# Performance work log

Measured on AMD Instinct MI355X. Metric: run time of the kernel, lower is better.

## Reference

```python
import jax, jax.numpy as jnp
import numpy as np

N, E, G = 50000, 400000, 2000
H, HEADS, HD = 128, 4, 32


def setup_inputs() -> dict:
    key = jax.random.key(0)
    ks = jax.random.split(key, 16)
    nrm = lambda k, shape, s=0.05: jax.random.normal(k, shape, dtype=jnp.float32) * s
    inp = {}
    inp["x"] = jax.random.normal(ks[0], (N, 39), dtype=jnp.float32)
    inp["edge_index"] = jax.random.randint(ks[1], (2, E), 0, N, dtype=jnp.int32)
    inp["edge_attr"] = jax.random.normal(ks[2], (E, 8), dtype=jnp.float32)
    inp["batch"] = jnp.sort(jax.random.randint(ks[3], (N,), 0, G, dtype=jnp.int32))
    inp["in_W"] = nrm(ks[4], (39, H)); inp["in_b"] = jnp.zeros((H,), jnp.float32)
    inp["in_g"] = jnp.ones((H,), jnp.float32); inp["in_beta"] = jnp.zeros((H,), jnp.float32)
    inp["Wl"] = nrm(ks[5], (3, H, H)); inp["Wr"] = nrm(ks[6], (3, H, H))
    inp["We"] = nrm(ks[7], (3, 8, H)); inp["att"] = nrm(ks[8], (3, HEADS, HD))
    inp["conv_b"] = jnp.zeros((3, H), jnp.float32)
    inp["bn_g"] = jnp.ones((3, H), jnp.float32); inp["bn_b"] = jnp.zeros((3, H), jnp.float32)
    inp["t1_W"] = nrm(ks[9], (3 * H, 256)); inp["t1_b"] = jnp.zeros((256,), jnp.float32)
    inp["t1_g"] = jnp.ones((256,), jnp.float32); inp["t1_beta"] = jnp.zeros((256,), jnp.float32)
    inp["t2_W"] = nrm(ks[10], (256, 128)); inp["t2_b"] = jnp.zeros((128,), jnp.float32)
    inp["t2_g"] = jnp.ones((128,), jnp.float32); inp["t2_beta"] = jnp.zeros((128,), jnp.float32)
    inp["head_W"] = nrm(ks[11], (128, 12)); inp["head_b"] = jnp.zeros((12,), jnp.float32)
    return inp


def _bn(h, g, b):
    # BatchNorm1d in training mode: normalize with batch statistics.
    m = h.mean(0)
    v = ((h - m) ** 2).mean(0)
    return g * (h - m) * jax.lax.rsqrt(v + 1e-5) + b


def reference(x, edge_index, edge_attr, batch, in_W, in_b, in_g, in_beta,
              Wl, Wr, We, att, conv_b, bn_g, bn_b,
              t1_W, t1_b, t1_g, t1_beta, t2_W, t2_b, t2_g, t2_beta,
              head_W, head_b):
    src, dst = edge_index[0], edge_index[1]  # messages flow src -> dst (PyG convention)
    xn = jax.nn.relu(_bn(x @ in_W + in_b, in_g, in_beta))  # [N, H]
    for l in range(3):  # three residual GATv2 layers
        xl = (xn @ Wl[l]).reshape(N, HEADS, HD)  # lin_l (source transform)
        xr = (xn @ Wr[l]).reshape(N, HEADS, HD)  # lin_r (target transform)
        ep = (edge_attr @ We[l]).reshape(E, HEADS, HD)
        m = jax.nn.leaky_relu(xl[src] + xr[dst] + ep, 0.2)  # [E, HEADS, HD]
        alpha = jnp.einsum('ehd,hd->eh', m, att[l])  # [E, HEADS]
        amax = jax.ops.segment_max(alpha, dst, num_segments=N)
        amax = jnp.where(jnp.isfinite(amax), amax, 0.0)  # nodes with no in-edges
        ae = jnp.exp(alpha - amax[dst])
        denom = jax.ops.segment_sum(ae, dst, num_segments=N)
        a = ae / (denom[dst] + 1e-16)  # scatter-softmax over neighborhoods
        agg = jax.ops.segment_sum(xl[src] * a[:, :, None], dst, num_segments=N)
        h = agg.reshape(N, H) + conv_b[l]
        h = jax.nn.elu(_bn(h, bn_g[l], bn_b[l]))
        xn = xn + h
    # 3-way global pooling per graph
    cnt = jax.ops.segment_sum(jnp.ones((N,), jnp.float32), batch, num_segments=G)
    sadd = jax.ops.segment_sum(xn, batch, num_segments=G)
    smean = sadd / jnp.maximum(cnt, 1.0)[:, None]
    smax = jax.ops.segment_max(xn, batch, num_segments=G)
    smax = jnp.where(cnt[:, None] > 0, smax, 0.0)
    xg = jnp.concatenate([smean, smax, sadd], axis=1)  # [G, 3H]
    t = jax.nn.relu(_bn(xg @ t1_W + t1_b, t1_g, t1_beta))
    t = jax.nn.relu(_bn(t @ t2_W + t2_b, t2_g, t2_beta))
    return jax.nn.sigmoid(t @ head_W + head_b)  # [G, 12]
```

## Files before the change

### kernel.cpp

```cpp
#include <hip/hip_runtime.h>
#include <math.h>


constexpr int N_ = 50000;
constexpr int E_ = 400000;
constexpr int G_ = 2000;
constexpr int H_ = 128;
constexpr int IN_ = 39;

typedef __attribute__((ext_vector_type(8))) short bf16x8;
typedef __attribute__((ext_vector_type(4))) float f32x4;

__device__ __forceinline__ unsigned pk_bf16(float a, float b) {
  unsigned ua = __float_as_uint(a);
  unsigned ub = __float_as_uint(b);
  ua = (ua + 0x7fffu + ((ua >> 16) & 1u)) >> 16;
  ub = (ub + 0x7fffu + ((ub >> 16) & 1u)) & 0xffff0000u;
  return ua | ub;
}
__device__ __forceinline__ unsigned short bf16_1(float x) {
  unsigned u = __float_as_uint(x);
  u = (u + 0x7fffu + ((u >> 16) & 1u)) >> 16;
  return (unsigned short)u;
}
__device__ __forceinline__ float up_lo(unsigned u) { return __uint_as_float(u << 16); }
__device__ __forceinline__ float up_hi(unsigned u) { return __uint_as_float(u & 0xffff0000u); }

__global__ __launch_bounds__(256) void hist_kernel(const int* __restrict__ keys, int n,
                                                   int* __restrict__ cnt) {
  for (int i = blockIdx.x * 256 + threadIdx.x; i < n; i += gridDim.x * 256)
    atomicAdd(&cnt[keys[i]], 1);
}

__global__ __launch_bounds__(1024) void scan_local(const int* __restrict__ in,
                                                   int* __restrict__ outx,
                                                   int* __restrict__ bsum, int n) {
  __shared__ int wsum[16];
  int t = threadIdx.x, lane = t & 63, wid = t >> 6;
  int idx = blockIdx.x * 1024 + t;
  int v = (idx < n) ? in[idx] : 0;
  int x = v;
#pragma unroll
  for (int off = 1; off < 64; off <<= 1) {
    int y = __shfl_up(x, off, 64);
    if (lane >= off) x += y;
  }
  if (lane == 63) wsum[wid] = x;
  __syncthreads();
  if (t == 0) {
    int acc = 0;
#pragma unroll
    for (int w = 0; w < 16; w++) { int tmp = wsum[w]; wsum[w] = acc; acc += tmp; }
    bsum[blockIdx.x] = acc;
  }
  __syncthreads();
  if (idx < n) outx[idx] = wsum[wid] + x - v;
}

__global__ __launch_bounds__(64) void scan_bsum(const int* __restrict__ bsum,
                                                int* __restrict__ boff, int nb) {
  int t = threadIdx.x;
  int v = (t < nb) ? bsum[t] : 0;
  int x = v;
#pragma unroll
  for (int off = 1; off < 64; off <<= 1) {
    int y = __shfl_up(x, off, 64);
    if (t >= off) x += y;
  }
  boff[t] = x - v;
}

__global__ __launch_bounds__(1024) void scan_add(int* __restrict__ eoff,
                                                 const int* __restrict__ boff,
                                                 int* __restrict__ cursor, int n) {
  int idx = blockIdx.x * 1024 + threadIdx.x;
  if (idx < n) {
    int e = eoff[idx] + boff[idx >> 10];
    eoff[idx] = e;
    cursor[idx] = e;
  }
  if (idx == 0) eoff[n] = E_;
}

__global__ __launch_bounds__(256) void goff_from_sorted(const int* __restrict__ batch,
                                                        int* __restrict__ goff) {
  int i = blockIdx.x * 256 + threadIdx.x;
  if (i >= N_) return;
  int bi = batch[i];
  int bp = (i == 0) ? -1 : batch[i - 1];
  for (int g = bp + 1; g <= bi; g++) goff[g] = i;
  if (i == N_ - 1) {
    for (int g = bi + 1; g <= G_; g++) goff[g] = N_;
  }
}

__global__ __launch_bounds__(256) void edge_scatter(const int* __restrict__ ei,
                                                    const float* __restrict__ ea,
                                                    int* __restrict__ cursor,
                                                    int* __restrict__ esrc,
                                                    unsigned* __restrict__ easb) {
  int e = blockIdx.x * 256 + threadIdx.x;
  if (e >= E_) return;
  int src = ei[e];
  int dst = ei[E_ + e];
  int j = atomicAdd(&cursor[dst], 1);
  esrc[j] = src;
  const float4* eav = (const float4*)(ea + (size_t)e * 8);
  float4 a0 = eav[0], a1 = eav[1];
  uint4 o;
  o.x = pk_bf16(a0.x, a0.y);
  o.y = pk_bf16(a0.z, a0.w);
  o.z = pk_bf16(a1.x, a1.y);
  o.w = pk_bf16(a1.z, a1.w);
  ((uint4*)easb)[j] = o;
}

__global__ __launch_bounds__(256) void pack_weights(const float* __restrict__ Wl,
                                                    const float* __restrict__ Wr,
                                                    unsigned short* __restrict__ wpack) {
  int i = blockIdx.x * 256 + threadIdx.x;
  if (i >= 3 * 128 * 256) return;
  int l = i >> 15;
  int rem = i & 32767;
  int k = rem >> 8;
  int n = rem & 255;
  const float* Wsrc = (n < 128) ? (Wl + l * H_ * H_) : (Wr + l * H_ * H_);
  int nn = n & 127;
  wpack[(size_t)l * 32768 + n * 128 + k] = bf16_1(Wsrc[k * H_ + nn]);
}

__global__ __launch_bounds__(256) void in_gemm(const float* __restrict__ x,
                                               const float* __restrict__ W,
                                               const float* __restrict__ b,
                                               float* __restrict__ y,
                                               float* __restrict__ ssum,
                                               float* __restrict__ ssq) {
  __shared__ float xs[32][40];
  __shared__ float s1[256], s2[256];
  int t = threadIdx.x;
  int row0 = blockIdx.x * 32;
  for (int i = t; i < 32 * IN_; i += 256) {
    int r = i / IN_, k = i % IN_;
    int row = row0 + r;
    xs[r][k] = (row < N_) ? x[row * IN_ + k] : 0.f;
  }
  __syncthreads();
  int col = t & 127;
  int half = t >> 7;
  float acc[16];
#pragma unroll
  for (int r = 0; r < 16; r++) acc[r] = 0.f;
  for (int k = 0; k < IN_; k++) {
    float w = W[k * H_ + col];
#pragma unroll
    for (int r = 0; r < 16; r++) acc[r] = fmaf(xs[half * 16 + r][k], w, acc[r]);
  }
  float bb = b[col];
  float a1 = 0.f, a2 = 0.f;
#pragma unroll
  for (int r = 0; r < 16; r++) {
    int row = row0 + half * 16 + r;
    float v = acc[r] + bb;
    if (row < N_) {
      y[row * H_ + col] = v;
      a1 += v;
      a2 = fmaf(v, v, a2);
    }
  }
  s1[t] = a1; s2[t] = a2;
  __syncthreads();
  if (t < 128) {
    atomicAdd(&ssum[t], s1[t] + s1[t + 128]);
    atomicAdd(&ssq[t], s2[t] + s2[t + 128]);
  }
}

template <int MODE>
__global__ __launch_bounds__(256) void gemm_mfma(float* __restrict__ xn,
                                                 const float* __restrict__ buf,
                                                 const float* __restrict__ g,
                                                 const float* __restrict__ beta,
                                                 const float* __restrict__ ssum,
                                                 const float* __restrict__ ssq,
                                                 float rows_inv,
                                                 const unsigned short* __restrict__ wp,
                                                 unsigned* __restrict__ xlb,
                                                 unsigned* __restrict__ xrb) {
  __shared__ char smem[17408 + 20480];
  short (*a_s)[136] = (short(*)[136])smem;
  short (*b_s)[40] = (short(*)[40])(smem + 17408);
  float* t2base = (float*)(smem + 17408);
  int t = threadIdx.x;
  int lane = t & 63, w = t >> 6;
  int quad = lane >> 4, lc = lane & 15;
  int row0 = blockIdx.x * 64;

  {
    int r = t >> 2;
    int row = row0 + r;
    int kb0 = (t & 3) * 32;
    bool valid = row < N_;
    for (int kk = 0; kk < 32; kk += 4) {
      int c = kb0 + kk;
      float4 v = make_float4(0.f, 0.f, 0.f, 0.f);
      if (valid) {
        float4 bv = *(const float4*)&buf[(size_t)row * H_ + c];
        float4 gv = *(const float4*)&g[c];
        float4 be = *(const float4*)&beta[c];
        float4 s1 = *(const float4*)&ssum[c];
        float4 s2 = *(const float4*)&ssq[c];
        float m0 = s1.x * rows_inv, m1 = s1.y * rows_inv, m2 = s1.z * rows_inv, m3 = s1.w * rows_inv;
        float r0 = rsqrtf(s2.x * rows_inv - m0 * m0 + 1e-5f);
        float r1 = rsqrtf(s2.y * rows_inv - m1 * m1 + 1e-5f);
        float r2 = rsqrtf(s2.z * rows_inv - m2 * m2 + 1e-5f);
        float r3 = rsqrtf(s2.w * rows_inv - m3 * m3 + 1e-5f);
        float t0 = gv.x * (bv.x - m0) * r0 + be.x;
        float t1 = gv.y * (bv.y - m1) * r1 + be.y;
        float t2 = gv.z * (bv.z - m2) * r2 + be.z;
        float t3 = gv.w * (bv.w - m3) * r3 + be.w;
        if (MODE == 1) {
          v = make_float4(fmaxf(t0, 0.f), fmaxf(t1, 0.f), fmaxf(t2, 0.f), fmaxf(t3, 0.f));
        } else {
          float4 xo = *(const float4*)&xn[(size_t)row * H_ + c];
          v.x = xo.x + ((t0 > 0.f) ? t0 : (__expf(t0) - 1.f));
          v.y = xo.y + ((t1 > 0.f) ? t1 : (__expf(t1) - 1.f));
          v.z = xo.z + ((t2 > 0.f) ? t2 : (__expf(t2) - 1.f));
          v.w = xo.w + ((t3 > 0.f) ? t3 : (__expf(t3) - 1.f));
        }
        *(float4*)&xn[(size_t)row * H_ + c] = v;
      }
      uint2 pk;
      pk.x = pk_bf16(v.x, v.y);
      pk.y = pk_bf16(v.z, v.w);
      *(uint2*)&a_s[r][c] = pk;
    }
  }

  f32x4 acc[16];
#pragma unroll
  for (int nt = 0; nt < 16; nt++) acc[nt] = (f32x4){0.f, 0.f, 0.f, 0.f};

  for (int kb = 0; kb < 4; kb++) {
    __syncthreads();
    for (int i = t; i < 1024; i += 256) {
      int n = i >> 2;
      int k8 = (i & 3) * 8;
      *(uint4*)&b_s[n][k8] = *(const uint4*)&wp[(size_t)n * 128 + kb * 32 + k8];
    }
    __syncthreads();
    bf16x8 av = *(const bf16x8*)&a_s[w * 16 + lc][kb * 32 + quad * 8];
#pragma unroll
    for (int nt = 0; nt < 16; nt++) {
      bf16x8 bv = *(const bf16x8*)&b_s[nt * 16 + lc][quad * 8];
      acc[nt] = __builtin_amdgcn_mfma_f32_16x16x32_bf16(av, bv, acc[nt], 0, 0, 0);
    }
  }
  __syncthreads();

  float* t2 = t2base + w * 544;
  for (int ntp = 0; ntp < 8; ntp++) {
#pragma unroll
    for (int rr = 0; rr < 4; rr++) {
      t2[(quad * 4 + rr) * 34 + lc] = acc[2 * ntp][rr];
      t2[(quad * 4 + rr) * 34 + 16 + lc] = acc[2 * ntp + 1][rr];
    }
    __asm__ volatile("s_waitcnt lgkmcnt(0)" ::: "memory");
#pragma unroll
    for (int it = 0; it < 4; it++) {
      int item = lane + it * 64;
      int p = item & 15, rowi = item >> 4;
      float v0 = t2[rowi * 34 + 2 * p];
      float v1 = t2[rowi * 34 + 2 * p + 1];
      unsigned u = pk_bf16(v0, v1);
      int colpair = ntp * 16 + p;
      int rowg = row0 + w * 16 + rowi;
      if (rowg < N_) {
        if (colpair < 64) xlb[(size_t)rowg * 64 + colpair] = u;
        else xrb[(size_t)rowg * 64 + colpair - 64] = u;
      }
    }
    __asm__ volatile("s_waitcnt lgkmcnt(0)" ::: "memory");
  }
}

__device__ __forceinline__ float ep8u(const uint4& u, const float* w) {
  float ep = up_lo(u.x) * w[0];
  ep = fmaf(up_hi(u.x), w[1], ep);
  ep = fmaf(up_lo(u.y), w[2], ep);
  ep = fmaf(up_hi(u.y), w[3], ep);
  ep = fmaf(up_lo(u.z), w[4], ep);
  ep = fmaf(up_hi(u.z), w[5], ep);
  ep = fmaf(up_lo(u.w), w[6], ep);
  ep = fmaf(up_hi(u.w), w[7], ep);
  return ep;
}

__global__ __launch_bounds__(256) void agg_csr(const int* __restrict__ eoff,
                                               const int* __restrict__ esrc,
                                               const unsigned* __restrict__ easb,
                                               const float* __restrict__ Wel,
                                               const float* __restrict__ attl,
                                               const unsigned* __restrict__ xlb,
                                               const unsigned* __restrict__ xrb,
                                               const float* __restrict__ cb,
                                               float* __restrict__ buf,
                                               float* __restrict__ ssum,
                                               float* __restrict__ ssq) {
  __shared__ float sA[256], sB[256], sC[256], sD[256];
  int t = threadIdx.x;
  int l = t & 63;
  int sub = t >> 6;
  int c0 = l * 2;
  float w0[8], w1[8];
#pragma unroll
  for (int k = 0; k < 8; k++) {
    float2 wv = *(const float2*)&Wel[k * H_ + c0];
    w0[k] = wv.x; w1[k] = wv.y;
  }
  float2 attv = *(const float2*)&attl[c0];
  float2 cbv = *(const float2*)&cb[c0];
  const uint4* eas4 = (const uint4*)easb;
  float a1_0 = 0.f, a1_1 = 0.f, a2_0 = 0.f, a2_1 = 0.f;
  for (int n = blockIdx.x * 4 + sub; n < N_; n += gridDim.x * 4) {
    unsigned xru = xrb[(size_t)n * 64 + l];
    float xr0 = up_lo(xru), xr1 = up_hi(xru);
    int e0 = eoff[n], e1 = eoff[n + 1];
    float acc0 = 0.f, acc1 = 0.f, den = 0.f;
    int j = e0;
    for (; j + 4 <= e1; j += 4) {
      int s0 = esrc[j], s1 = esrc[j + 1], s2 = esrc[j + 2], s3 = esrc[j + 3];
      uint4 u0 = eas4[j], u1 = eas4[j + 1], u2 = eas4[j + 2], u3 = eas4[j + 3];
      unsigned xu0 = xlb[(size_t)s0 * 64 + l];
      unsigned xu1 = xlb[(size_t)s1 * 64 + l];
      unsigned xu2 = xlb[(size_t)s2 * 64 + l];
      unsigned xu3 = xlb[(size_t)s3 * 64 + l];
      float x00 = up_lo(xu0), x01 = up_hi(xu0);
      float x10 = up_lo(xu1), x11 = up_hi(xu1);
      float x20 = up_lo(xu2), x21 = up_hi(xu2);
      float x30 = up_lo(xu3), x31 = up_hi(xu3);
      float m00 = x00 + xr0 + ep8u(u0, w0);
      float m01 = x01 + xr1 + ep8u(u0, w1);
      float m10 = x10 + xr0 + ep8u(u1, w0);
      float m11 = x11 + xr1 + ep8u(u1, w1);
      float m20 = x20 + xr0 + ep8u(u2, w0);
      float m21 = x21 + xr1 + ep8u(u2, w1);
      float m30 = x30 + xr0 + ep8u(u3, w0);
      float m31 = x31 + xr1 + ep8u(u3, w1);
      m00 = (m00 > 0.f) ? m00 : 0.2f * m00;
      m01 = (m01 > 0.f) ? m01 : 0.2f * m01;
      m10 = (m10 > 0.f) ? m10 : 0.2f * m10;
      m11 = (m11 > 0.f) ? m11 : 0.2f * m11;
      m20 = (m20 > 0.f) ? m20 : 0.2f * m20;
      m21 = (m21 > 0.f) ? m21 : 0.2f * m21;
      m30 = (m30 > 0.f) ? m30 : 0.2f * m30;
      m31 = (m31 > 0.f) ? m31 : 0.2f * m31;
      float p0 = fmaf(m00, attv.x, m01 * attv.y);
      float p1 = fmaf(m10, attv.x, m11 * attv.y);
      float p2 = fmaf(m20, attv.x, m21 * attv.y);
      float p3 = fmaf(m30, attv.x, m31 * attv.y);
#pragma unroll
      for (int off = 8; off > 0; off >>= 1) {
        p0 += __shfl_xor(p0, off, 64);
        p1 += __shfl_xor(p1, off, 64);
        p2 += __shfl_xor(p2, off, 64);
        p3 += __shfl_xor(p3, off, 64);
      }
      float e0v = __expf(p0), e1v = __expf(p1), e2v = __expf(p2), e3v = __expf(p3);
      acc0 = fmaf(e0v, x00, acc0); acc1 = fmaf(e0v, x01, acc1);
      acc0 = fmaf(e1v, x10, acc0); acc1 = fmaf(e1v, x11, acc1);
      acc0 = fmaf(e2v, x20, acc0); acc1 = fmaf(e2v, x21, acc1);
      acc0 = fmaf(e3v, x30, acc0); acc1 = fmaf(e3v, x31, acc1);
      den += (e0v + e1v) + (e2v + e3v);
    }
    for (; j < e1; j++) {
      int s0 = esrc[j];
      uint4 u0 = eas4[j];
      unsigned xu0 = xlb[(size_t)s0 * 64 + l];
      float x00 = up_lo(xu0), x01 = up_hi(xu0);
      float m00 = x00 + xr0 + ep8u(u0, w0);
      float m01 = x01 + xr1 + ep8u(u0, w1);
      m00 = (m00 > 0.f) ? m00 : 0.2f * m00;
      m01 = (m01 > 0.f) ? m01 : 0.2f * m01;
      float p0 = fmaf(m00, attv.x, m01 * attv.y);
#pragma unroll
      for (int off = 8; off > 0; off >>= 1) p0 += __shfl_xor(p0, off, 64);
      float e0v = __expf(p0);
      acc0 = fmaf(e0v, x00, acc0);
      acc1 = fmaf(e0v, x01, acc1);
      den += e0v;
    }
    float inv = 1.f / (den + 1e-16f);
    float h0 = acc0 * inv + cbv.x;
    float h1 = acc1 * inv + cbv.y;
    *(float2*)&buf[(size_t)n * H_ + c0] = make_float2(h0, h1);
    a1_0 += h0; a1_1 += h1;
    a2_0 = fmaf(h0, h0, a2_0); a2_1 = fmaf(h1, h1, a2_1);
  }
  sA[t] = a1_0; sB[t] = a1_1; sC[t] = a2_0; sD[t] = a2_1;
  __syncthreads();
  if (t < 64) {
    float r1 = sA[t] + sA[t + 64] + sA[t + 128] + sA[t + 192];
    float r2 = sB[t] + sB[t + 64] + sB[t + 128] + sB[t + 192];
    float r3 = sC[t] + sC[t + 64] + sC[t + 128] + sC[t + 192];
    float r4 = sD[t] + sD[t + 64] + sD[t + 128] + sD[t + 192];
    atomicAdd(&ssum[2 * t], r1);
    atomicAdd(&ssum[2 * t + 1], r2);
    atomicAdd(&ssq[2 * t], r3);
    atomicAdd(&ssq[2 * t + 1], r4);
  }
}

__global__ __launch_bounds__(256) void apply_bn_relu(const float* __restrict__ y,
                                                     float* __restrict__ out,
                                                     const float* __restrict__ g,
                                                     const float* __restrict__ beta,
                                                     const float* __restrict__ ssum,
                                                     const float* __restrict__ ssq,
                                                     float rows_inv,
                                                     long total, int cmask) {
  long i = (long)blockIdx.x * 256 + threadIdx.x;
  if (i >= total) return;
  int c = (int)i & cmask;
  float m = ssum[c] * rows_inv;
  float rs = rsqrtf(ssq[c] * rows_inv - m * m + 1e-5f);
  float v = g[c] * (y[i] - m) * rs + beta[c];
  out[i] = fmaxf(v, 0.f);
}

__global__ __launch_bounds__(128) void pool_residual(const int* __restrict__ goff,
                                                     const float* __restrict__ xn,
                                                     const float* __restrict__ buf,
                                                     const float* __restrict__ g,
                                                     const float* __restrict__ beta,
                                                     const float* __restrict__ ssum,
                                                     const float* __restrict__ ssq,
                                                     float rows_inv,
                                                     float* __restrict__ xg) {
  int gr = blockIdx.x;
  int t = threadIdx.x;
  int n0 = goff[gr], n1 = goff[gr + 1];
  float mm = ssum[t] * rows_inv;
  float rr = rsqrtf(ssq[t] * rows_inv - mm * mm + 1e-5f);
  float gg = g[t], bb = beta[t];
  float s = 0.f, mx = -INFINITY;
  for (int n = n0; n < n1; n++) {
    float w = gg * (buf[(size_t)n * H_ + t] - mm) * rr + bb;
    w = (w > 0.f) ? w : (__expf(w) - 1.f);
    float v = xn[(size_t)n * H_ + t] + w;
    s += v;
    mx = fmaxf(mx, v);
  }
  float c = (float)(n1 - n0);
  xg[gr * 384 + t] = s / fmaxf(c, 1.f);
  xg[gr * 384 + 128 + t] = (c > 0.f) ? mx : 0.f;
  xg[gr * 384 + 256 + t] = s;
}

template <int K, int COLS>
__global__ void mlp_gemm(const float* __restrict__ A, const float* __restrict__ W,
                         const float* __restrict__ b, float* __restrict__ Y, int rows,
                         float* __restrict__ ssum, float* __restrict__ ssq) {
  __shared__ float xs[8][K];
  int t = threadIdx.x;
  int row0 = blockIdx.x * 8;
  for (int i = t; i < 8 * K; i += COLS) {
    int r = i / K, k = i % K;
    int row = row0 + r;
    xs[r][k] = (row < rows) ? A[row * K + k] : 0.f;
  }
  __syncthreads();
  float acc[8];
#pragma unroll
  for (int r = 0; r < 8; r++) acc[r] = 0.f;
  for (int k = 0; k < K; k++) {
    float w = W[k * COLS + t];
#pragma unroll
    for (int r = 0; r < 8; r++) acc[r] = fmaf(xs[r][k], w, acc[r]);
  }
  float bb = b[t];
  float a1 = 0.f, a2 = 0.f;
#pragma unroll
  for (int r = 0; r < 8; r++) {
    int row = row0 + r;
    if (row < rows) {
      float v = acc[r] + bb;
      Y[row * COLS + t] = v;
      a1 += v;
      a2 = fmaf(v, v, a2);
    }
  }
  atomicAdd(&ssum[t], a1);
  atomicAdd(&ssq[t], a2);
}

__global__ __launch_bounds__(64) void head_kernel(const float* __restrict__ u,
                                                  const float* __restrict__ W,
                                                  const float* __restrict__ b,
                                                  float* __restrict__ out) {
  __shared__ float row[128];
  int g = blockIdx.x;
  int t = threadIdx.x;
  row[t] = u[g * 128 + t];
  row[t + 64] = u[g * 128 + 64 + t];
  __syncthreads();
  if (t < 12) {
    float acc = b[t];
    for (int k = 0; k < 128; k++) acc = fmaf(row[k], W[k * 12 + t], acc);
    out[g * 12 + t] = 1.f / (1.f + expf(-acc));
  }
}

extern "C" void kernel_launch(void* const* d_in, const int* in_sizes, int n_in, void* d_out,
                              int out_size, void* d_ws, size_t ws_size, hipStream_t stream) {
  (void)in_sizes; (void)n_in; (void)out_size; (void)ws_size;
  const float* x       = (const float*)d_in[0];
  const int*   ei      = (const int*)d_in[1];
  const float* ea      = (const float*)d_in[2];
  const int*   batch   = (const int*)d_in[3];
  const float* in_W    = (const float*)d_in[4];
  const float* in_b    = (const float*)d_in[5];
  const float* in_g    = (const float*)d_in[6];
  const float* in_beta = (const float*)d_in[7];
  const float* Wl      = (const float*)d_in[8];
  const float* Wr      = (const float*)d_in[9];
  const float* We      = (const float*)d_in[10];
  const float* att     = (const float*)d_in[11];
  const float* conv_b  = (const float*)d_in[12];
  const float* bn_g    = (const float*)d_in[13];
  const float* bn_b    = (const float*)d_in[14];
  const float* t1_W    = (const float*)d_in[15];
  const float* t1_b    = (const float*)d_in[16];
  const float* t1_g    = (const float*)d_in[17];
  const float* t1_beta = (const float*)d_in[18];
  const float* t2_W    = (const float*)d_in[19];
  const float* t2_b    = (const float*)d_in[20];
  const float* t2_g    = (const float*)d_in[21];
  const float* t2_beta = (const float*)d_in[22];
  const float* head_W  = (const float*)d_in[23];
  const float* head_b  = (const float*)d_in[24];
  float* out = (float*)d_out;

  float* p = (float*)d_ws;
  float* xn    = p; p += N_ * H_;
  float* buf   = p; p += N_ * H_;
  float* sstat = p; p += 6 * 512;
  float* xg    = p; p += G_ * 384;
  float* u1    = p; p += G_ * 256;
  float* u2    = p; p += G_ * 128;
  unsigned* up = (unsigned*)p;
  unsigned* xlb  = up; up += (size_t)N_ * 64;
  unsigned* xrb  = up; up += (size_t)N_ * 64;
  unsigned* easb = up; up += (size_t)E_ * 4;
  unsigned short* wpack = (unsigned short*)up; up += 3 * 32768 / 2;
  int* ip = (int*)up;
  int* deg    = ip; ip += N_;
  int* eoff   = ip; ip += N_ + 1;
  int* cursor = ip; ip += N_;
  int* goff   = ip; ip += G_ + 1;
  int* esrc   = ip; ip += E_;
  int* bsum   = ip; ip += 64;
  int* boff   = ip; ip += 64;

#define SSUM(s) (sstat + (s) * 512)
#define SSQ(s)  (sstat + (s) * 512 + 256)

  hipMemsetAsync(deg, 0, (size_t)N_ * sizeof(int), stream);
  hipMemsetAsync(sstat, 0, 6 * 512 * sizeof(float), stream);
  hist_kernel<<<1024, 256, 0, stream>>>(ei + E_, E_, deg);
  scan_local<<<49, 1024, 0, stream>>>(deg, eoff, bsum, N_);
  scan_bsum<<<1, 64, 0, stream>>>(bsum, boff, 49);
  scan_add<<<49, 1024, 0, stream>>>(eoff, boff, cursor, N_);
  edge_scatter<<<(E_ + 255) / 256, 256, 0, stream>>>(ei, ea, cursor, esrc, easb);
  goff_from_sorted<<<(N_ + 255) / 256, 256, 0, stream>>>(batch, goff);
  pack_weights<<<384, 256, 0, stream>>>(Wl, Wr, wpack);

  in_gemm<<<(N_ + 31) / 32, 256, 0, stream>>>(x, in_W, in_b, buf, SSUM(0), SSQ(0));

  const float rnInv = 1.f / N_;
  for (int l = 0; l < 3; l++) {
    if (l == 0) {
      gemm_mfma<1><<<782, 256, 0, stream>>>(xn, buf, in_g, in_beta, SSUM(0), SSQ(0), rnInv,
                                            wpack + (size_t)l * 32768, xlb, xrb);
    } else {
      gemm_mfma<2><<<782, 256, 0, stream>>>(xn, buf, bn_g + (l - 1) * H_, bn_b + (l - 1) * H_,
                                            SSUM(l), SSQ(l), rnInv,
                                            wpack + (size_t)l * 32768, xlb, xrb);
    }
    agg_csr<<<2048, 256, 0, stream>>>(eoff, esrc, easb, We + l * 8 * H_, att + l * H_,
                                      xlb, xrb, conv_b + l * H_, buf, SSUM(l + 1), SSQ(l + 1));
  }

  pool_residual<<<G_, 128, 0, stream>>>(goff, xn, buf, bn_g + 2 * H_, bn_b + 2 * H_,
                                        SSUM(3), SSQ(3), rnInv, xg);

  const float rgInv = 1.f / G_;
  mlp_gemm<384, 256><<<G_ / 8, 256, 0, stream>>>(xg, t1_W, t1_b, u1, G_, SSUM(4), SSQ(4));
  apply_bn_relu<<<(G_ * 256 + 255) / 256, 256, 0, stream>>>(u1, u1, t1_g, t1_beta,
                                                            SSUM(4), SSQ(4), rgInv,
                                                            (long)G_ * 256, 255);

  mlp_gemm<256, 128><<<G_ / 8, 128, 0, stream>>>(u1, t2_W, t2_b, u2, G_, SSUM(5), SSQ(5));
  apply_bn_relu<<<(G_ * 128 + 255) / 256, 256, 0, stream>>>(u2, u2, t2_g, t2_beta,
                                                            SSUM(5), SSQ(5), rgInv,
                                                            (long)G_ * 128, 127);

  head_kernel<<<G_, 64, 0, stream>>>(u2, head_W, head_b, out);
#undef SSUM
#undef SSQ
}
```

Before: 853.7 us.

## Prefetch CSR metadata across nodes and batch edge gathers via wave-wide readlane

After: 871.6 us. 1.02x slower.

```diff
diff --git a/kernel.cpp b/kernel.cpp
--- a/kernel.cpp
+++ b/kernel.cpp
@@ -283,7 +283,7 @@
   }
 }
 
-__device__ __forceinline__ float ep8u(const uint4& u, const float* w) {
+__device__ __forceinline__ float ep8u(const uint4& u, const float (&w)[8]) {
   float ep = up_lo(u.x) * w[0];
   ep = fmaf(up_hi(u.x), w[1], ep);
   ep = fmaf(up_lo(u.y), w[2], ep);
@@ -293,6 +293,56 @@
   ep = fmaf(up_lo(u.w), w[6], ep);
   ep = fmaf(up_hi(u.w), w[7], ep);
   return ep;
+}
+
+template <int W, bool MASK>
+__device__ __forceinline__ void edge_pack(int spre, int j, int cnt, int base, int l,
+                                          const unsigned* __restrict__ xlb,
+                                          const uint4* __restrict__ eas4,
+                                          float xr0, float xr1,
+                                          const float (&w0)[8], const float (&w1)[8],
+                                          float2 attv,
+                                          float& acc0, float& acc1, float& den) {
+  int ss[W];
+  unsigned xu[W];
+  uint4 u[W];
+#pragma unroll
+  for (int q = 0; q < W; q++) {
+    int idx = j + q;
+    int cl = MASK ? ((idx < cnt) ? idx : (cnt - 1)) : idx;
+    ss[q] = __builtin_amdgcn_readlane(spre, cl);
+  }
+#pragma unroll
+  for (int q = 0; q < W; q++) xu[q] = xlb[(size_t)ss[q] * 64 + l];
+#pragma unroll
+  for (int q = 0; q < W; q++) {
+    int idx = j + q;
+    int cl = MASK ? ((idx < cnt) ? idx : (cnt - 1)) : idx;
+    u[q] = eas4[base + cl];
+  }
+  float p[W], x0[W], x1[W];
+#pragma unroll
+  for (int q = 0; q < W; q++) {
+    x0[q] = up_lo(xu[q]);
+    x1[q] = up_hi(xu[q]);
+    float m0 = x0[q] + xr0 + ep8u(u[q], w0);
+    float m1 = x1[q] + xr1 + ep8u(u[q], w1);
+    m0 = (m0 > 0.f) ? m0 : 0.2f * m0;
+    m1 = (m1 > 0.f) ? m1 : 0.2f * m1;
+    p[q] = fmaf(m0, attv.x, m1 * attv.y);
+  }
+#pragma unroll
+  for (int off = 8; off > 0; off >>= 1)
+#pragma unroll
+    for (int q = 0; q < W; q++) p[q] += __shfl_xor(p[q], off, 64);
+#pragma unroll
+  for (int q = 0; q < W; q++) {
+    float ev = __expf(p[q]);
+    if (MASK && (j + q >= cnt)) ev = 0.f;
+    acc0 = fmaf(ev, x0[q], acc0);
+    acc1 = fmaf(ev, x1[q], acc1);
+    den += ev;
+  }
 }
 
 __global__ __launch_bounds__(256) void agg_csr(const int* __restrict__ eoff,
@@ -321,81 +371,69 @@
   float2 cbv = *(const float2*)&cb[c0];
   const uint4* eas4 = (const uint4*)easb;
   float a1_0 = 0.f, a1_1 = 0.f, a2_0 = 0.f, a2_1 = 0.f;
-  for (int n = blockIdx.x * 4 + sub; n < N_; n += gridDim.x * 4) {
-    unsigned xru = xrb[(size_t)n * 64 + l];
+
+  const int stride = gridDim.x * 4;
+  int n0 = blockIdx.x * 4 + sub;
+
+  int cur_e0 = 0, cur_e1 = 0, cur_spre = 0;
+  unsigned cur_xr = 0;
+  int nx_e0 = 0, nx_e1 = 0;
+  unsigned nx_xr = 0;
+  if (n0 < N_) {
+    cur_e0 = eoff[n0];
+    cur_e1 = eoff[n0 + 1];
+    cur_xr = xrb[(size_t)n0 * 64 + l];
+    cur_spre = (cur_e0 + l < cur_e1) ? esrc[cur_e0 + l] : 0;
+    int n1 = n0 + stride;
+    if (n1 < N_) {
+      nx_e0 = eoff[n1];
+      nx_e1 = eoff[n1 + 1];
+      nx_xr = xrb[(size_t)n1 * 64 + l];
+    }
+  }
+
+  for (int n = n0; n < N_; n += stride) {
+    int e0 = cur_e0, e1 = cur_e1, spre = cur_spre;
+    unsigned xru = cur_xr;
+    int n1 = n + stride;
+    int n2 = n + 2 * stride;
+
+    int nspre = 0;
+    if (n1 < N_) nspre = (nx_e0 + l < nx_e1) ? esrc[nx_e0 + l] : 0;
+    int n2_e0 = 0, n2_e1 = 0;
+    unsigned n2_xr = 0;
+    if (n2 < N_) {
+      n2_e0 = eoff[n2];
+      n2_e1 = eoff[n2 + 1];
+      n2_xr = xrb[(size_t)n2 * 64 + l];
+    }
+
     float xr0 = up_lo(xru), xr1 = up_hi(xru);
-    int e0 = eoff[n], e1 = eoff[n + 1];
     float acc0 = 0.f, acc1 = 0.f, den = 0.f;
-    int j = e0;
-    for (; j + 4 <= e1; j += 4) {
-      int s0 = esrc[j], s1 = esrc[j + 1], s2 = esrc[j + 2], s3 = esrc[j + 3];
-      uint4 u0 = eas4[j], u1 = eas4[j + 1], u2 = eas4[j + 2], u3 = eas4[j + 3];
-      unsigned xu0 = xlb[(size_t)s0 * 64 + l];
-      unsigned xu1 = xlb[(size_t)s1 * 64 + l];
-      unsigned xu2 = xlb[(size_t)s2 * 64 + l];
-      unsigned xu3 = xlb[(size_t)s3 * 64 + l];
-      float x00 = up_lo(xu0), x01 = up_hi(xu0);
-      float x10 = up_lo(xu1), x11 = up_hi(xu1);
-      float x20 = up_lo(xu2), x21 = up_hi(xu2);
-      float x30 = up_lo(xu3), x31 = up_hi(xu3);
-      float m00 = x00 + xr0 + ep8u(u0, w0);
-      float m01 = x01 + xr1 + ep8u(u0, w1);
-      float m10 = x10 + xr0 + ep8u(u1, w0);
-      float m11 = x11 + xr1 + ep8u(u1, w1);
-      float m20 = x20 + xr0 + ep8u(u2, w0);
-      float m21 = x21 + xr1 + ep8u(u2, w1);
-      float m30 = x30 + xr0 + ep8u(u3, w0);
-      float m31 = x31 + xr1 + ep8u(u3, w1);
-      m00 = (m00 > 0.f) ? m00 : 0.2f * m00;
-      m01 = (m01 > 0.f) ? m01 : 0.2f * m01;
-      m10 = (m10 > 0.f) ? m10 : 0.2f * m10;
-      m11 = (m11 > 0.f) ? m11 : 0.2f * m11;
-      m20 = (m20 > 0.f) ? m20 : 0.2f * m20;
-      m21 = (m21 > 0.f) ? m21 : 0.2f * m21;
-      m30 = (m30 > 0.f) ? m30 : 0.2f * m30;
-      m31 = (m31 > 0.f) ? m31 : 0.2f * m31;
-      float p0 = fmaf(m00, attv.x, m01 * attv.y);
-      float p1 = fmaf(m10, attv.x, m11 * attv.y);
-      float p2 = fmaf(m20, attv.x, m21 * attv.y);
-      float p3 = fmaf(m30, attv.x, m31 * attv.y);
-#pragma unroll
-      for (int off = 8; off > 0; off >>= 1) {
-        p0 += __shfl_xor(p0, off, 64);
-        p1 += __shfl_xor(p1, off, 64);
-        p2 += __shfl_xor(p2, off, 64);
-        p3 += __shfl_xor(p3, off, 64);
-      }
-      float e0v = __expf(p0), e1v = __expf(p1), e2v = __expf(p2), e3v = __expf(p3);
-      acc0 = fmaf(e0v, x00, acc0); acc1 = fmaf(e0v, x01, acc1);
-      acc0 = fmaf(e1v, x10, acc0); acc1 = fmaf(e1v, x11, acc1);
-      acc0 = fmaf(e2v, x20, acc0); acc1 = fmaf(e2v, x21, acc1);
-      acc0 = fmaf(e3v, x30, acc0); acc1 = fmaf(e3v, x31, acc1);
-      den += (e0v + e1v) + (e2v + e3v);
-    }
-    for (; j < e1; j++) {
-      int s0 = esrc[j];
-      uint4 u0 = eas4[j];
-      unsigned xu0 = xlb[(size_t)s0 * 64 + l];
-      float x00 = up_lo(xu0), x01 = up_hi(xu0);
-      float m00 = x00 + xr0 + ep8u(u0, w0);
-      float m01 = x01 + xr1 + ep8u(u0, w1);
-      m00 = (m00 > 0.f) ? m00 : 0.2f * m00;
-      m01 = (m01 > 0.f) ? m01 : 0.2f * m01;
-      float p0 = fmaf(m00, attv.x, m01 * attv.y);
-#pragma unroll
-      for (int off = 8; off > 0; off >>= 1) p0 += __shfl_xor(p0, off, 64);
-      float e0v = __expf(p0);
-      acc0 = fmaf(e0v, x00, acc0);
-      acc1 = fmaf(e0v, x01, acc1);
-      den += e0v;
-    }
+
+    for (int base = e0; base < e1; base += 64) {
+      int cnt = min(64, e1 - base);
+      if (base != e0) spre = (base + l < e1) ? esrc[base + l] : 0;
+      int j = 0;
+      for (; j + 8 <= cnt; j += 8)
+        edge_pack<8, false>(spre, j, cnt, base, l, xlb, eas4, xr0, xr1, w0, w1, attv,
+                            acc0, acc1, den);
+      for (; j < cnt; j += 4)
+        edge_pack<4, true>(spre, j, cnt, base, l, xlb, eas4, xr0, xr1, w0, w1, attv,
+                           acc0, acc1, den);
+    }
+
     float inv = 1.f / (den + 1e-16f);
     float h0 = acc0 * inv + cbv.x;
     float h1 = acc1 * inv + cbv.y;
     *(float2*)&buf[(size_t)n * H_ + c0] = make_float2(h0, h1);
     a1_0 += h0; a1_1 += h1;
     a2_0 = fmaf(h0, h0, a2_0); a2_1 = fmaf(h1, h1, a2_1);
-  }
+
+    cur_e0 = nx_e0; cur_e1 = nx_e1; cur_xr = nx_xr; cur_spre = nspre;
+    nx_e0 = n2_e0; nx_e1 = n2_e1; nx_xr = n2_xr;
+  }
+
   sA[t] = a1_0; sB[t] = a1_1; sC[t] = a2_0; sD[t] = a2_1;
   __syncthreads();
   if (t < 64) {
```
